# Kernel tuning notes

Hardware: AMD Instinct MI355X
Metric: run time of the kernel (lower is better)

The kernel has to match this reference:

```python
import jax, jax.numpy as jnp
import numpy as np

A, D, F = 2048, 64, 12  # atoms, depth, filter_length


def _chemconv(x, conn, bond, filters):
    # x: (A, D); conn: (A, A, F); bond: (A, F, 2); filters: (D, F, D+2)
    # node_connection = conn.transpose(1,2) @ x -> (A, F, D)
    ncon = jnp.einsum('anf,nd->afd', conn, x)
    combined = jnp.concatenate([ncon, bond], axis=2)  # (A, F, D+2)
    # broadcast-multiply by filters then sum over last two dims -> (A, out_depth)
    return jnp.einsum('afc,ofc->ao', combined, filters)


def setup_inputs() -> dict:
    key = jax.random.key(0)
    k1, k2, k3, k4, k5 = jax.random.split(key, 5)
    x = jax.random.normal(k1, (A, D), dtype=jnp.float32)
    conn = jax.random.uniform(k2, (A, A, F), dtype=jnp.float32)
    bond = jax.random.normal(k3, (A, F, 2), dtype=jnp.float32)
    scale = 1.0 / D  # filters.data.normal_() * (1/in_depth)
    f0 = jax.random.normal(k4, (D, F, D + 2), dtype=jnp.float32) * scale
    f1 = jax.random.normal(k5, (D, F, D + 2), dtype=jnp.float32) * scale
    return {
        'node_property_tensor': x,
        'connectivity_tensor': conn,
        'bond_property_tensor': bond,
        'filters0': f0,
        'filters1': f1,
    }


def reference(node_property_tensor, connectivity_tensor, bond_property_tensor, filters0, filters1):
    x = node_property_tensor
    out = x
    for filt in (filters0, filters1):
        # each ChemConv layer is applied twice (same weights), per the torch code
        out = jax.nn.relu(_chemconv(out, connectivity_tensor, bond_property_tensor, filt))
        out = _chemconv(out, connectivity_tensor, bond_property_tensor, filt)
        out = out + x  # residual to the original block input
        out = jax.nn.relu(out)
    return out
```

## Files before the change

### kernel.cpp

```cpp
#include <hip/hip_runtime.h>


#define A_N 2048
#define D_N 64
#define F_N 12
#define K_TOTAL (A_N * F_N)
#define NSPLIT 32
#define KSEG (K_TOTAL / NSPLIT)
#define BK 64
#define NKB (KSEG / BK)

typedef short short8 __attribute__((ext_vector_type(8)));
typedef float f32x16 __attribute__((ext_vector_type(16)));

#define GLOAD16(ldsp, gp)                                                        \
  __builtin_amdgcn_global_load_lds(                                              \
      (const __attribute__((address_space(1))) void*)(gp),                       \
      (__attribute__((address_space(3))) void*)(ldsp), 16, 0, 0)

__device__ __forceinline__ unsigned pk_bf16(float a, float b) {
  unsigned ua = __float_as_uint(a);
  unsigned ub = __float_as_uint(b);
  ua += 0x7fffu + ((ua >> 16) & 1u);
  ub += 0x7fffu + ((ub >> 16) & 1u);
  return (ua >> 16) | (ub & 0xffff0000u);
}

__device__ __forceinline__ unsigned short bf16_1(float v) {
  unsigned u = __float_as_uint(v);
  u += 0x7fffu + ((u >> 16) & 1u);
  return (unsigned short)(u >> 16);
}

__global__ void k_prep(const float* __restrict__ x, float* __restrict__ xt,
                       const float* __restrict__ bond, const float* __restrict__ f0,
                       const float* __restrict__ f1, float* __restrict__ bt0,
                       float* __restrict__ bt1) {
  int t = threadIdx.x;
  if (blockIdx.x < 32) {
    __shared__ float ld[64][65];
    int m0 = blockIdx.x * 64;
    int r = t >> 2, cq = (t & 3) * 16;
    const float4* src = (const float4*)(x + (size_t)(m0 + r) * 64 + cq);
#pragma unroll
    for (int i = 0; i < 4; ++i) {
      float4 v = src[i];
      ld[r][cq + i * 4 + 0] = v.x;
      ld[r][cq + i * 4 + 1] = v.y;
      ld[r][cq + i * 4 + 2] = v.z;
      ld[r][cq + i * 4 + 3] = v.w;
    }
    __syncthreads();
    int c = t >> 2, ml0 = (t & 3) * 16;
    float4* dst = (float4*)(xt + (size_t)c * 2048 + m0 + ml0);
#pragma unroll
    for (int i = 0; i < 4; ++i) {
      float4 v;
      v.x = ld[ml0 + i * 4 + 0][c];
      v.y = ld[ml0 + i * 4 + 1][c];
      v.z = ld[ml0 + i * 4 + 2][c];
      v.w = ld[ml0 + i * 4 + 3][c];
      dst[i] = v;
    }
  } else {
    int b = blockIdx.x - 32;
    int a = (b & 31) * 64 + (t & 63);
    int o = (b >> 5) * 4 + (t >> 6);
    float s0 = 0.f, s1 = 0.f;
#pragma unroll
    for (int f = 0; f < F_N; ++f) {
#pragma unroll
      for (int j = 0; j < 2; ++j) {
        float bv = bond[a * 24 + f * 2 + j];
        s0 += bv * f0[o * 792 + f * 66 + 64 + j];
        s1 += bv * f1[o * 792 + f * 66 + 64 + j];
      }
    }
    bt0[o * 2048 + a] = s0;
    bt1[o * 2048 + a] = s1;
  }
}

__global__ void k_g(const float* __restrict__ vt, const float* __restrict__ filt,
                    unsigned short* __restrict__ gtt) {
  __shared__ float W[12][64];
  int o = blockIdx.y;
  int t = threadIdx.x;
  for (int i = t; i < 768; i += 256) W[i >> 6][i & 63] = filt[o * 792 + (i >> 6) * 66 + (i & 63)];
  __syncthreads();
  int n = blockIdx.x * 256 + t;
  float acc[12] = {0.f, 0.f, 0.f, 0.f, 0.f, 0.f, 0.f, 0.f, 0.f, 0.f, 0.f, 0.f};
#pragma unroll 4
  for (int d = 0; d < 64; ++d) {
    float v = vt[d * 2048 + n];
#pragma unroll
    for (int f = 0; f < F_N; ++f) acc[f] += v * W[f][d];
  }
  int kbase = n * 12;
#pragma unroll
  for (int f = 0; f < F_N; ++f) {
    int k = kbase + f;
    int q = k >> 6, c = k & 63;
    gtt[(size_t)q * 4096 + o * 64 + c] = bf16_1(acc[f]);
  }
}

__launch_bounds__(256, 3)
__global__ void k_big1(const float* __restrict__ conn, const unsigned short* __restrict__ gtt,
                       unsigned short* __restrict__ connt, float* __restrict__ part) {
  __shared__ __align__(16) unsigned short smem[24576];
  int t = threadIdx.x, lane = t & 63, w = t >> 6;
  int atile = blockIdx.x, ks = blockIdx.y;
  const float* cs0 = conn + (size_t)atile * 128 * K_TOTAL + ks * KSEG;
  unsigned short* tile = connt + (size_t)(atile * NSPLIT + ks) * (NKB * 8192);
  const unsigned short* gs = gtt + (size_t)ks * (NKB * 4096);

  int q0 = w * 64 + lane;
  int gOff[8], lOff[8];
#pragma unroll
  for (int s = 0; s < 8; ++s) {
    int q = q0 + s * 256;
    int row = q >> 4, c16 = q & 15, c = c16 >> 1;
    gOff[s] = row * K_TOTAL + c16 * 4;
    lOff[s] = row * 64 + ((c ^ (row & 7)) << 3) + ((c16 & 1) << 2);
  }

  int rl = lane >> 3, sl = lane & 7;
  int csz = sl ^ rl;
  int gSrc[2];
  unsigned short* gDst[2];
#pragma unroll
  for (int j = 0; j < 2; ++j) {
    gSrc[j] = (w * 16 + j * 8 + rl) * 64 + csz * 8;
    gDst[j] = smem + 16384 + (w * 16 + j * 8) * 64;
  }

  f32x16 acc0, acc1;
#pragma unroll
  for (int i = 0; i < 16; ++i) { acc0[i] = 0.f; acc1[i] = 0.f; }

  int oh = w >> 1, ah = w & 1;
  int orow = oh * 32 + (lane & 31);
  int arow = ah * 64 + (lane & 31);
  int sw = lane & 7;
  int khalf = lane >> 5;

  float4 rg[8];
#pragma unroll
  for (int s = 0; s < 8; ++s) rg[s] = *(const float4*)(cs0 + gOff[s]);
  GLOAD16(gDst[0], gs + gSrc[0]);
  GLOAD16(gDst[1], gs + gSrc[1]);

  for (int kb = 0; kb < NKB; ++kb) {
    unsigned short* cb = smem + (kb & 1) * 8192;
    uint2* tb = (uint2*)tile + kb * 2048;
#pragma unroll
    for (int s = 0; s < 8; ++s) {
      uint2 p;
      p.x = pk_bf16(rg[s].x, rg[s].y);
      p.y = pk_bf16(rg[s].z, rg[s].w);
      *(uint2*)(cb + lOff[s]) = p;
      tb[q0 + s * 256] = p;
    }
    __syncthreads();
    if (kb + 1 < NKB) {
      int b = (kb + 1) & 1;
      GLOAD16(gDst[0] + b * 4096, gs + (kb + 1) * 4096 + gSrc[0]);
      GLOAD16(gDst[1] + b * 4096, gs + (kb + 1) * 4096 + gSrc[1]);
      const float* nsrc = cs0 + (kb + 1) * 64;
#pragma unroll
      for (int s = 0; s < 8; ++s) rg[s] = *(const float4*)(nsrc + gOff[s]);
    }
    const unsigned short* gb = smem + 16384 + (kb & 1) * 4096;
#pragma unroll
    for (int kk = 0; kk < 4; ++kk) {
      int c = kk * 2 + khalf;
      int coff = ((c ^ sw) << 3);
      short8 af = *(const short8*)(gb + orow * 64 + coff);
      short8 b0 = *(const short8*)(cb + arow * 64 + coff);
      short8 b1 = *(const short8*)(cb + (arow + 32) * 64 + coff);
      acc0 = __builtin_amdgcn_mfma_f32_32x32x16_bf16(af, b0, acc0, 0, 0, 0);
      acc1 = __builtin_amdgcn_mfma_f32_32x32x16_bf16(af, b1, acc1, 0, 0, 0);
    }
  }

  float* pp = part + (size_t)ks * (64 * 2048);
  int a0 = atile * 128 + ah * 64 + (lane & 31);
  int ob = oh * 32 + 4 * khalf;
#pragma unroll
  for (int rg2 = 0; rg2 < 16; ++rg2) {
    int o = ob + (rg2 & 3) + 8 * (rg2 >> 2);
    pp[o * 2048 + a0] = acc0[rg2];
    pp[o * 2048 + a0 + 32] = acc1[rg2];
  }
}

__launch_bounds__(256, 3)
__global__ void k_big(const unsigned short* __restrict__ connt,
                      const unsigned short* __restrict__ gtt, float* __restrict__ part) {
  __shared__ __align__(16) unsigned short smem[24576];
  int t = threadIdx.x, lane = t & 63, w = t >> 6;
  int atile = blockIdx.x, ks = blockIdx.y;
  const unsigned short* ct = connt + (size_t)(atile * NSPLIT + ks) * (NKB * 8192);
  const unsigned short* gs = gtt + (size_t)ks * (NKB * 4096);

  int rl = lane >> 3, sl = lane & 7;
  int cs = sl ^ rl;

  int cSrc[4], gSrc[2];
  unsigned short *cDst[4], *gDst[2];
#pragma unroll
  for (int j = 0; j < 4; ++j) {
    cSrc[j] = (w * 32 + j * 8 + rl) * 64 + cs * 8;
    cDst[j] = smem + (w * 32 + j * 8) * 64;
  }
#pragma unroll
  for (int j = 0; j < 2; ++j) {
    gSrc[j] = (w * 16 + j * 8 + rl) * 64 + cs * 8;
    gDst[j] = smem + 16384 + (w * 16 + j * 8) * 64;
  }

  f32x16 acc0, acc1;
#pragma unroll
  for (int i = 0; i < 16; ++i) { acc0[i] = 0.f; acc1[i] = 0.f; }

  int oh = w >> 1, ah = w & 1;
  int orow = oh * 32 + (lane & 31);
  int arow = ah * 64 + (lane & 31);
  int sw = lane & 7;
  int khalf = lane >> 5;

#pragma unroll
  for (int j = 0; j < 4; ++j) GLOAD16(cDst[j], ct + cSrc[j]);
#pragma unroll
  for (int j = 0; j < 2; ++j) GLOAD16(gDst[j], gs + gSrc[j]);

  for (int kb = 0; kb < NKB; ++kb) {
    __syncthreads();
    if (kb + 1 < NKB) {
      int b = (kb + 1) & 1;
      int co = (kb + 1) * 8192, go = (kb + 1) * 4096;
#pragma unroll
      for (int j = 0; j < 4; ++j) GLOAD16(cDst[j] + b * 8192, ct + co + cSrc[j]);
#pragma unroll
      for (int j = 0; j < 2; ++j) GLOAD16(gDst[j] + b * 4096, gs + go + gSrc[j]);
    }
    const unsigned short* cb = smem + (kb & 1) * 8192;
    const unsigned short* gb = smem + 16384 + (kb & 1) * 4096;
#pragma unroll
    for (int kk = 0; kk < 4; ++kk) {
      int c = kk * 2 + khalf;
      int coff = ((c ^ sw) << 3);
      short8 af = *(const short8*)(gb + orow * 64 + coff);
      short8 b0 = *(const short8*)(cb + arow * 64 + coff);
      short8 b1 = *(const short8*)(cb + (arow + 32) * 64 + coff);
      acc0 = __builtin_amdgcn_mfma_f32_32x32x16_bf16(af, b0, acc0, 0, 0, 0);
      acc1 = __builtin_amdgcn_mfma_f32_32x32x16_bf16(af, b1, acc1, 0, 0, 0);
    }
  }

  float* pp = part + (size_t)ks * (64 * 2048);
  int a0 = atile * 128 + ah * 64 + (lane & 31);
  int ob = oh * 32 + 4 * khalf;
#pragma unroll
  for (int rg = 0; rg < 16; ++rg) {
    int o = ob + (rg & 3) + 8 * (rg >> 2);
    pp[o * 2048 + a0] = acc0[rg];
    pp[o * 2048 + a0 + 32] = acc1[rg];
  }
}

__global__ void k_reduce(const float* __restrict__ part, const float* __restrict__ bt,
                         const float* __restrict__ xt, float* __restrict__ curt,
                         float* __restrict__ outp, int residual, int final_layer) {
  int i4 = blockIdx.x * 256 + threadIdx.x;
  float4 s = ((const float4*)bt)[i4];
#pragma unroll
  for (int sI = 0; sI < NSPLIT; ++sI) {
    float4 p = ((const float4*)part)[(size_t)sI * 32768 + i4];
    s.x += p.x; s.y += p.y; s.z += p.z; s.w += p.w;
  }
  if (residual) {
    float4 r = ((const float4*)xt)[i4];
    s.x += r.x; s.y += r.y; s.z += r.z; s.w += r.w;
  }
  s.x = fmaxf(s.x, 0.f); s.y = fmaxf(s.y, 0.f);
  s.z = fmaxf(s.z, 0.f); s.w = fmaxf(s.w, 0.f);
  ((float4*)curt)[i4] = s;
  if (final_layer) {
    int idx = i4 * 4;
    int o = idx >> 11, m = idx & 2047;
    outp[(m + 0) * 64 + o] = s.x;
    outp[(m + 1) * 64 + o] = s.y;
    outp[(m + 2) * 64 + o] = s.z;
    outp[(m + 3) * 64 + o] = s.w;
  }
}

extern "C" void kernel_launch(void* const* d_in, const int* in_sizes, int n_in,
                              void* d_out, int out_size, void* d_ws, size_t ws_size,
                              hipStream_t stream) {
  const float* x    = (const float*)d_in[0];
  const float* conn = (const float*)d_in[1];
  const float* bond = (const float*)d_in[2];
  const float* f0   = (const float*)d_in[3];
  const float* f1   = (const float*)d_in[4];
  float* out = (float*)d_out;

  char* ws = (char*)d_ws;
  float* xt   = (float*)(ws + 0);
  float* curt = (float*)(ws + 524288);
  float* bt0  = (float*)(ws + 1048576);
  float* bt1  = (float*)(ws + 1572864);
  unsigned short* gtt = (unsigned short*)(ws + 2097152);
  float* part = (float*)(ws + 5242880);
  unsigned short* connt = (unsigned short*)(ws + 33554432);

  k_prep<<<544, 256, 0, stream>>>(x, xt, bond, f0, f1, bt0, bt1);

  for (int layer = 0; layer < 4; ++layer) {
    const float* filt = (layer < 2) ? f0 : f1;
    const float* bt   = (layer < 2) ? bt0 : bt1;
    const float* vin  = (layer == 0) ? xt : curt;
    k_g<<<dim3(8, 64), 256, 0, stream>>>(vin, filt, gtt);
    if (layer == 0)
      k_big1<<<dim3(16, NSPLIT), 256, 0, stream>>>(conn, gtt, connt, part);
    else
      k_big<<<dim3(16, NSPLIT), 256, 0, stream>>>(connt, gtt, part);
    k_reduce<<<128, 256, 0, stream>>>(part, bt, xt, curt, out, layer & 1, layer == 3);
  }
}
```

Before: 472.2 us.

## Split conn conversion into own kernel and triple-buffer k_big loads

Moves the fp32-to-bf16 conversion of the connectivity tensor out of the first-layer GEMM into a separate k_cvt kernel, so all four layers use the same k_big. k_big now uses a three-stage LDS ring with explicit vmcnt waits, prefetching two blocks ahead to hide global load latency. Launch bounds drop to 2 blocks per CU to fit the larger LDS footprint. k_g computes two atoms per thread with transposed, vectorised weight reads. The trade-off is lower occupancy and an extra full pass over conn in k_cvt.

```diff
diff --git a/kernel.cpp b/kernel.cpp
--- a/kernel.cpp
+++ b/kernel.cpp
@@ -17,6 +17,8 @@
   __builtin_amdgcn_global_load_lds(                                              \
       (const __attribute__((address_space(1))) void*)(gp),                       \
       (__attribute__((address_space(3))) void*)(ldsp), 16, 0, 0)
+
+#define VMWAIT(n) asm volatile("s_waitcnt vmcnt(" #n ")" ::: "memory")
 
 __device__ __forceinline__ unsigned pk_bf16(float a, float b) {
   unsigned ua = __float_as_uint(a);
@@ -81,58 +83,89 @@
   }
 }
 
+__global__ void k_cvt(const float* __restrict__ conn, unsigned short* __restrict__ connt) {
+  int t = threadIdx.x;
+  int kb = blockIdx.x, ks = blockIdx.y, atile = blockIdx.z;
+  const float* src = conn + (size_t)(atile * 128) * K_TOTAL + ks * KSEG + kb * 64;
+  unsigned short* dst = connt + (size_t)((atile * NSPLIT + ks) * NKB + kb) * 8192;
+  int r0 = t >> 3, c0 = (t & 7) * 8;
+#pragma unroll
+  for (int i = 0; i < 4; ++i) {
+    int row = r0 + i * 32;
+    const float4* s4 = (const float4*)(src + (size_t)row * K_TOTAL + c0);
+    float4 a = s4[0], b = s4[1];
+    uint4 p;
+    p.x = pk_bf16(a.x, a.y);
+    p.y = pk_bf16(a.z, a.w);
+    p.z = pk_bf16(b.x, b.y);
+    p.w = pk_bf16(b.z, b.w);
+    *(uint4*)(dst + row * 64 + c0) = p;
+  }
+}
+
 __global__ void k_g(const float* __restrict__ vt, const float* __restrict__ filt,
                     unsigned short* __restrict__ gtt) {
-  __shared__ float W[12][64];
+  __shared__ __align__(16) float WT[64][12];
   int o = blockIdx.y;
   int t = threadIdx.x;
-  for (int i = t; i < 768; i += 256) W[i >> 6][i & 63] = filt[o * 792 + (i >> 6) * 66 + (i & 63)];
+  for (int i = t; i < 768; i += 256) {
+    int d = i / 12, f = i % 12;
+    WT[d][f] = filt[o * 792 + f * 66 + d];
+  }
   __syncthreads();
-  int n = blockIdx.x * 256 + t;
-  float acc[12] = {0.f, 0.f, 0.f, 0.f, 0.f, 0.f, 0.f, 0.f, 0.f, 0.f, 0.f, 0.f};
+  int n0 = blockIdx.x * 512 + t;
+  float acc0[12], acc1[12];
+#pragma unroll
+  for (int f = 0; f < 12; ++f) { acc0[f] = 0.f; acc1[f] = 0.f; }
 #pragma unroll 4
   for (int d = 0; d < 64; ++d) {
-    float v = vt[d * 2048 + n];
-#pragma unroll
-    for (int f = 0; f < F_N; ++f) acc[f] += v * W[f][d];
-  }
-  int kbase = n * 12;
+    float v0 = vt[d * 2048 + n0];
+    float v1 = vt[d * 2048 + n0 + 256];
+    const float4* wp = (const float4*)WT[d];
+    float4 w0 = wp[0], w1 = wp[1], w2 = wp[2];
+    acc0[0] += v0 * w0.x;  acc0[1] += v0 * w0.y;  acc0[2]  += v0 * w0.z;  acc0[3]  += v0 * w0.w;
+    acc0[4] += v0 * w1.x;  acc0[5] += v0 * w1.y;  acc0[6]  += v0 * w1.z;  acc0[7]  += v0 * w1.w;
+    acc0[8] += v0 * w2.x;  acc0[9] += v0 * w2.y;  acc0[10] += v0 * w2.z;  acc0[11] += v0 * w2.w;
+    acc1[0] += v1 * w0.x;  acc1[1] += v1 * w0.y;  acc1[2]  += v1 * w0.z;  acc1[3]  += v1 * w0.w;
+    acc1[4] += v1 * w1.x;  acc1[5] += v1 * w1.y;  acc1[6]  += v1 * w1.z;  acc1[7]  += v1 * w1.w;
+    acc1[8] += v1 * w2.x;  acc1[9] += v1 * w2.y;  acc1[10] += v1 * w2.z;  acc1[11] += v1 * w2.w;
+  }
+  int kb0 = n0 * 12;
 #pragma unroll
   for (int f = 0; f < F_N; ++f) {
-    int k = kbase + f;
-    int q = k >> 6, c = k & 63;
-    gtt[(size_t)q * 4096 + o * 64 + c] = bf16_1(acc[f]);
-  }
-}
-
-__launch_bounds__(256, 3)
-__global__ void k_big1(const float* __restrict__ conn, const unsigned short* __restrict__ gtt,
-                       unsigned short* __restrict__ connt, float* __restrict__ part) {
-  __shared__ __align__(16) unsigned short smem[24576];
+    int k = kb0 + f;
+    gtt[(size_t)(k >> 6) * 4096 + o * 64 + (k & 63)] = bf16_1(acc0[f]);
+  }
+  int kb1 = (n0 + 256) * 12;
+#pragma unroll
+  for (int f = 0; f < F_N; ++f) {
+    int k = kb1 + f;
+    gtt[(size_t)(k >> 6) * 4096 + o * 64 + (k & 63)] = bf16_1(acc1[f]);
+  }
+}
+
+__launch_bounds__(256, 2)
+__global__ void k_big(const unsigned short* __restrict__ connt,
+                      const unsigned short* __restrict__ gtt, float* __restrict__ part) {
+  __shared__ __align__(16) unsigned short smem[36864];
   int t = threadIdx.x, lane = t & 63, w = t >> 6;
   int atile = blockIdx.x, ks = blockIdx.y;
-  const float* cs0 = conn + (size_t)atile * 128 * K_TOTAL + ks * KSEG;
-  unsigned short* tile = connt + (size_t)(atile * NSPLIT + ks) * (NKB * 8192);
+  const unsigned short* ct = connt + (size_t)(atile * NSPLIT + ks) * (NKB * 8192);
   const unsigned short* gs = gtt + (size_t)ks * (NKB * 4096);
 
-  int q0 = w * 64 + lane;
-  int gOff[8], lOff[8];
-#pragma unroll
-  for (int s = 0; s < 8; ++s) {
-    int q = q0 + s * 256;
-    int row = q >> 4, c16 = q & 15, c = c16 >> 1;
-    gOff[s] = row * K_TOTAL + c16 * 4;
-    lOff[s] = row * 64 + ((c ^ (row & 7)) << 3) + ((c16 & 1) << 2);
-  }
-
   int rl = lane >> 3, sl = lane & 7;
-  int csz = sl ^ rl;
-  int gSrc[2];
-  unsigned short* gDst[2];
+  int cs = sl ^ rl;
+
+  int cSrc[4], gSrc[2], cDst[4], gDst[2];
+#pragma unroll
+  for (int j = 0; j < 4; ++j) {
+    cSrc[j] = (w * 32 + j * 8 + rl) * 64 + cs * 8;
+    cDst[j] = (w * 32 + j * 8) * 64;
+  }
 #pragma unroll
   for (int j = 0; j < 2; ++j) {
-    gSrc[j] = (w * 16 + j * 8 + rl) * 64 + csz * 8;
-    gDst[j] = smem + 16384 + (w * 16 + j * 8) * 64;
+    gSrc[j] = (w * 16 + j * 8 + rl) * 64 + cs * 8;
+    gDst[j] = 8192 + (w * 16 + j * 8) * 64;
   }
 
   f32x16 acc0, acc1;
@@ -145,108 +178,30 @@
   int sw = lane & 7;
   int khalf = lane >> 5;
 
-  float4 rg[8];
-#pragma unroll
-  for (int s = 0; s < 8; ++s) rg[s] = *(const float4*)(cs0 + gOff[s]);
-  GLOAD16(gDst[0], gs + gSrc[0]);
-  GLOAD16(gDst[1], gs + gSrc[1]);
-
+#pragma unroll
+  for (int p = 0; p < 2; ++p) {
+    unsigned short* base = smem + p * 12288;
+#pragma unroll
+    for (int j = 0; j < 4; ++j) GLOAD16(base + cDst[j], ct + p * 8192 + cSrc[j]);
+#pragma unroll
+    for (int j = 0; j < 2; ++j) GLOAD16(base + gDst[j], gs + p * 4096 + gSrc[j]);
+  }
+
+#pragma unroll
   for (int kb = 0; kb < NKB; ++kb) {
-    unsigned short* cb = smem + (kb & 1) * 8192;
-    uint2* tb = (uint2*)tile + kb * 2048;
-#pragma unroll
-    for (int s = 0; s < 8; ++s) {
-      uint2 p;
-      p.x = pk_bf16(rg[s].x, rg[s].y);
-      p.y = pk_bf16(rg[s].z, rg[s].w);
-      *(uint2*)(cb + lOff[s]) = p;
-      tb[q0 + s * 256] = p;
-    }
-    __syncthreads();
-    if (kb + 1 < NKB) {
-      int b = (kb + 1) & 1;
-      GLOAD16(gDst[0] + b * 4096, gs + (kb + 1) * 4096 + gSrc[0]);
-      GLOAD16(gDst[1] + b * 4096, gs + (kb + 1) * 4096 + gSrc[1]);
-      const float* nsrc = cs0 + (kb + 1) * 64;
-#pragma unroll
-      for (int s = 0; s < 8; ++s) rg[s] = *(const float4*)(nsrc + gOff[s]);
-    }
-    const unsigned short* gb = smem + 16384 + (kb & 1) * 4096;
-#pragma unroll
-    for (int kk = 0; kk < 4; ++kk) {
-      int c = kk * 2 + khalf;
-      int coff = ((c ^ sw) << 3);
-      short8 af = *(const short8*)(gb + orow * 64 + coff);
-      short8 b0 = *(const short8*)(cb + arow * 64 + coff);
-      short8 b1 = *(const short8*)(cb + (arow + 32) * 64 + coff);
-      acc0 = __builtin_amdgcn_mfma_f32_32x32x16_bf16(af, b0, acc0, 0, 0, 0);
-      acc1 = __builtin_amdgcn_mfma_f32_32x32x16_bf16(af, b1, acc1, 0, 0, 0);
-    }
-  }
-
-  float* pp = part + (size_t)ks * (64 * 2048);
-  int a0 = atile * 128 + ah * 64 + (lane & 31);
-  int ob = oh * 32 + 4 * khalf;
-#pragma unroll
-  for (int rg2 = 0; rg2 < 16; ++rg2) {
-    int o = ob + (rg2 & 3) + 8 * (rg2 >> 2);
-    pp[o * 2048 + a0] = acc0[rg2];
-    pp[o * 2048 + a0 + 32] = acc1[rg2];
-  }
-}
-
-__launch_bounds__(256, 3)
-__global__ void k_big(const unsigned short* __restrict__ connt,
-                      const unsigned short* __restrict__ gtt, float* __restrict__ part) {
-  __shared__ __align__(16) unsigned short smem[24576];
-  int t = threadIdx.x, lane = t & 63, w = t >> 6;
-  int atile = blockIdx.x, ks = blockIdx.y;
-  const unsigned short* ct = connt + (size_t)(atile * NSPLIT + ks) * (NKB * 8192);
-  const unsigned short* gs = gtt + (size_t)ks * (NKB * 4096);
-
-  int rl = lane >> 3, sl = lane & 7;
-  int cs = sl ^ rl;
-
-  int cSrc[4], gSrc[2];
-  unsigned short *cDst[4], *gDst[2];
-#pragma unroll
-  for (int j = 0; j < 4; ++j) {
-    cSrc[j] = (w * 32 + j * 8 + rl) * 64 + cs * 8;
-    cDst[j] = smem + (w * 32 + j * 8) * 64;
-  }
-#pragma unroll
-  for (int j = 0; j < 2; ++j) {
-    gSrc[j] = (w * 16 + j * 8 + rl) * 64 + cs * 8;
-    gDst[j] = smem + 16384 + (w * 16 + j * 8) * 64;
-  }
-
-  f32x16 acc0, acc1;
-#pragma unroll
-  for (int i = 0; i < 16; ++i) { acc0[i] = 0.f; acc1[i] = 0.f; }
-
-  int oh = w >> 1, ah = w & 1;
-  int orow = oh * 32 + (lane & 31);
-  int arow = ah * 64 + (lane & 31);
-  int sw = lane & 7;
-  int khalf = lane >> 5;
-
-#pragma unroll
-  for (int j = 0; j < 4; ++j) GLOAD16(cDst[j], ct + cSrc[j]);
-#pragma unroll
-  for (int j = 0; j < 2; ++j) GLOAD16(gDst[j], gs + gSrc[j]);
-
-  for (int kb = 0; kb < NKB; ++kb) {
-    __syncthreads();
-    if (kb + 1 < NKB) {
-      int b = (kb + 1) & 1;
-      int co = (kb + 1) * 8192, go = (kb + 1) * 4096;
-#pragma unroll
-      for (int j = 0; j < 4; ++j) GLOAD16(cDst[j] + b * 8192, ct + co + cSrc[j]);
-#pragma unroll
-      for (int j = 0; j < 2; ++j) GLOAD16(gDst[j] + b * 4096, gs + go + gSrc[j]);
-    }
-    const unsigned short* cb = smem + (kb & 1) * 8192;
-    const unsigned short* gb = smem + 16384 + (kb & 1) * 4096;
+    if (kb < NKB - 1) VMWAIT(6);
+    else VMWAIT(0);
+    __builtin_amdgcn_s_barrier();
+    asm volatile("" ::: "memory");
+    if (kb + 2 < NKB) {
+      unsigned short* base = smem + ((kb + 2) % 3) * 12288;
+#pragma unroll
+      for (int j = 0; j < 4; ++j) GLOAD16(base + cDst[j], ct + (kb + 2) * 8192 + cSrc[j]);
+#pragma unroll
+      for (int j = 0; j < 2; ++j) GLOAD16(base + gDst[j], gs + (kb + 2) * 4096 + gSrc[j]);
+    }
+    const unsigned short* cb = smem + (kb % 3) * 12288;
+    const unsigned short* gb = cb + 8192;
 #pragma unroll
     for (int kk = 0; kk < 4; ++kk) {
       int c = kk * 2 + khalf;
@@ -317,16 +272,14 @@
   unsigned short* connt = (unsigned short*)(ws + 33554432);
 
   k_prep<<<544, 256, 0, stream>>>(x, xt, bond, f0, f1, bt0, bt1);
+  k_cvt<<<dim3(NKB, NSPLIT, 16), 256, 0, stream>>>(conn, connt);
 
   for (int layer = 0; layer < 4; ++layer) {
     const float* filt = (layer < 2) ? f0 : f1;
     const float* bt   = (layer < 2) ? bt0 : bt1;
     const float* vin  = (layer == 0) ? xt : curt;
-    k_g<<<dim3(8, 64), 256, 0, stream>>>(vin, filt, gtt);
-    if (layer == 0)
-      k_big1<<<dim3(16, NSPLIT), 256, 0, stream>>>(conn, gtt, connt, part);
-    else
-      k_big<<<dim3(16, NSPLIT), 256, 0, stream>>>(connt, gtt, part);
+    k_g<<<dim3(4, 64), 256, 0, stream>>>(vin, filt, gtt);
+    k_big<<<dim3(16, NSPLIT), 256, 0, stream>>>(connt, gtt, part);
     k_reduce<<<128, 256, 0, stream>>>(part, bt, xt, curt, out, layer & 1, layer == 3);
   }
 }
```

New measurement: 458.2 us. 1.03x faster.
